# Kernel optimization log

Measured on AMD Instinct MI355X. Metric: run time of the kernel, lower is better.

Reference implementation:

```python
import jax, jax.numpy as jnp
from jax import lax
import numpy as np

NX, NQ, NU, B = 512, 512, 128, 32768
EPS = 1e-3
ALPHA = 0.0


def setup_inputs() -> dict:
    key = jax.random.key(0)
    ks = jax.random.split(key, 8)
    std = 1.0 / np.sqrt(NX)
    return {
        "t": jnp.zeros((1,), jnp.float32),
        "xi": jax.random.normal(ks[0], (B, NX), jnp.float32),
        "u": jax.random.normal(ks[1], (B, NU), jnp.float32),
        "Pstar": jax.random.normal(ks[2], (NX, NX), jnp.float32) * std,
        "Chi": jax.random.normal(ks[3], (NX, NQ), jnp.float32) * std,
        "Y1": jax.random.normal(ks[4], (NX, NX), jnp.float32) * std,
        "B2": jax.random.normal(ks[5], (NX, NU), jnp.float32) * std,
        "D12": jax.random.normal(ks[6], (NQ, NU), jnp.float32) * std,
        "X": jax.random.normal(ks[7], (NX + NQ, NX + NQ), jnp.float32) * std,
    }


def reference(t, xi, u, Pstar, Chi, Y1, B2, D12, X):
    # Parameter construction (direct parametrization of a contractive REN)
    P = 0.5 * (Pstar @ Pstar.T) + EPS * jnp.eye(NX, dtype=xi.dtype)
    H = X @ X.T + EPS * jnp.eye(NX + NQ, dtype=xi.dtype)
    H1 = H[:NX, :NX]          # [nx, nx]
    H2 = H[:NX, NX:]          # [nx, nq]
    H4 = H[NX:, NX:]          # [nq, nq]
    Y = -0.5 * (H1 + ALPHA * P + Y1 - Y1.T)
    lam = 0.5 * jnp.diagonal(H4)                 # Lambda = diag(lam)
    Pinv = jnp.linalg.inv(P)
    A = Pinv @ Y                                  # F.linear(inv(P), Y.T)
    D11 = -jnp.tril(H4, -1) / lam[:, None]        # strictly lower triangular
    C1 = Chi.T / lam[:, None]                     # [nq, nx]
    B1 = Pinv @ (-H2 - Chi)                       # [nx, nq]

    # Forward-substitution recurrence: w[:, i] = tanh(xi@C1[i] + w@D11[i] + u@D12[i])
    base = xi @ C1.T + u @ D12.T                  # [B, nq], bv = 0 (bias=False)

    def step(w, i):
        v = base[:, i] + w @ D11[i]               # [B]; D11[i, j>=i] == 0
        w = w.at[:, i].set(jnp.tanh(v))
        return w, None

    w0 = jnp.zeros((xi.shape[0], NQ), xi.dtype)
    w, _ = lax.scan(step, w0, jnp.arange(NQ))

    # xi_dot = A xi + B1 w + B2 u  (bx = 0 since bias=False)
    xi_ = xi @ A.T + w @ B1.T + u @ B2.T
    return xi_
```

## Files before the change

kernel.cpp:

```cpp
#include <hip/hip_runtime.h>
#include <hip/hip_bf16.h>
#include <cstdint>
#include <cstddef>

#define NXD 512
#define NQD 512
#define NUD 128
#define NBATCH 32768
#define EPSV 1e-3f
#define KBASE 640
#define KFIN 1152

typedef unsigned short u16;
typedef short bf16x8 __attribute__((ext_vector_type(8)));
typedef _Float16 f16x8 __attribute__((ext_vector_type(8)));
typedef float f32x4 __attribute__((ext_vector_type(4)));

__device__ __forceinline__ void gload_lds16(const u16* g, u16* l) {
  __builtin_amdgcn_global_load_lds((const __attribute__((address_space(1))) void*)g,
                                   (__attribute__((address_space(3))) void*)l, 16, 0, 0);
}

__device__ __forceinline__ float fast_tanh(float x) {
  float e = __expf(2.0f * x);
  return 1.0f - 2.0f / (e + 1.0f);
}

__device__ __forceinline__ void gbar(unsigned int* flags, unsigned int ep) {
  unsigned int* arr = flags;
  unsigned int* rel = flags + 4096;
  int tid = threadIdx.x, bid = blockIdx.x;
  __syncthreads();
  if (bid == 0) {
    if (tid == 0)
      __hip_atomic_store(&arr[0], ep, __ATOMIC_RELEASE, __HIP_MEMORY_SCOPE_AGENT);
    if (tid < 64) {
#pragma unroll
      for (int g = tid; g < 256; g += 64)
        while (__hip_atomic_load(&arr[g * 16], __ATOMIC_RELAXED, __HIP_MEMORY_SCOPE_AGENT) < ep)
          __builtin_amdgcn_s_sleep(4);
    }
    __threadfence();
    __syncthreads();
    if (tid < 64) {
#pragma unroll
      for (int g = tid; g < 256; g += 64)
        __hip_atomic_store(&rel[g * 16], ep, __ATOMIC_RELEASE, __HIP_MEMORY_SCOPE_AGENT);
    }
  } else {
    if (tid == 0) {
      __hip_atomic_store(&arr[bid * 16], ep, __ATOMIC_RELEASE, __HIP_MEMORY_SCOPE_AGENT);
      while (__hip_atomic_load(&rel[bid * 16], __ATOMIC_RELAXED, __HIP_MEMORY_SCOPE_AGENT) < ep)
        __builtin_amdgcn_s_sleep(4);
      __threadfence();
    }
    __syncthreads();
  }
}

template <int TA, int TB>
__device__ __forceinline__ void tile_mm(float acc[4][4], float* As, float* Bs,
                                        const float* A, int lda, int ai0, int ak0,
                                        const float* B, int ldb, int bj0, int bk0,
                                        int K) {
  int tid = threadIdx.x;
  int tx = tid & 15, ty = tid >> 4;
  for (int kc = 0; kc < K; kc += 16) {
    float4 av, bv;
    if (TA == 0) {
      int row = tid >> 2, q4 = (tid & 3) * 4;
      av = *(const float4*)&A[(size_t)(ai0 + row) * lda + ak0 + kc + q4];
    } else {
      int kr = tid >> 4, m4 = (tid & 15) * 4;
      av = *(const float4*)&A[(size_t)(ak0 + kc + kr) * lda + ai0 + m4];
    }
    if (TB == 0) {
      int kr = tid >> 4, j4 = (tid & 15) * 4;
      bv = *(const float4*)&B[(size_t)(bk0 + kc + kr) * ldb + bj0 + j4];
    } else {
      int row = tid >> 2, q4 = (tid & 3) * 4;
      bv = *(const float4*)&B[(size_t)(bj0 + row) * ldb + bk0 + kc + q4];
    }
    __syncthreads();
    if (TA == 0) {
      int row = tid >> 2, q4 = (tid & 3) * 4;
      As[(q4 + 0) * 68 + row] = av.x; As[(q4 + 1) * 68 + row] = av.y;
      As[(q4 + 2) * 68 + row] = av.z; As[(q4 + 3) * 68 + row] = av.w;
    } else {
      int kr = tid >> 4, m4 = (tid & 15) * 4;
      *(float4*)&As[kr * 68 + m4] = av;
    }
    if (TB == 0) {
      int kr = tid >> 4, j4 = (tid & 15) * 4;
      *(float4*)&Bs[kr * 68 + j4] = bv;
    } else {
      int row = tid >> 2, q4 = (tid & 3) * 4;
      Bs[(q4 + 0) * 68 + row] = bv.x; Bs[(q4 + 1) * 68 + row] = bv.y;
      Bs[(q4 + 2) * 68 + row] = bv.z; Bs[(q4 + 3) * 68 + row] = bv.w;
    }
    __syncthreads();
#pragma unroll
    for (int kk = 0; kk < 16; ++kk) {
      float a4[4], b4[4];
      *(float4*)a4 = *(const float4*)&As[kk * 68 + ty * 4];
      *(float4*)b4 = *(const float4*)&Bs[kk * 68 + tx * 4];
#pragma unroll
      for (int i = 0; i < 4; ++i)
#pragma unroll
        for (int j = 0; j < 4; ++j) acc[i][j] += a4[i] * b4[j];
    }
  }
}

__device__ void chol_diag64(float* Pm, int kb, float* cb2, float* Ls) {
  int tid = threadIdx.x;
  int ty = tid >> 4, tx = tid & 15;
  int base = kb * 64;
  float T[4][4];
#pragma unroll
  for (int rr = 0; rr < 4; ++rr)
#pragma unroll
    for (int cc = 0; cc < 4; ++cc)
      T[rr][cc] = Pm[(size_t)(base + ty * 4 + rr) * 512 + base + tx * 4 + cc];

  for (int c = 0; c < 64; ++c) {
    float* cb = cb2 + (c & 1) * 72;
    if (tx == (c >> 2)) {
      int cc = c & 3;
#pragma unroll
      for (int rr = 0; rr < 4; ++rr) cb[ty * 4 + rr] = T[rr][cc];
    }
    __syncthreads();
    float dcv = cb[c];
    float dc = sqrtf(dcv);
    float rdc = 1.0f / dc;
    float rdcv = 1.0f / dcv;
    if (tx == (c >> 2)) {
      int cc = c & 3;
#pragma unroll
      for (int rr = 0; rr < 4; ++rr) {
        int r = ty * 4 + rr;
        if (r == c) T[rr][cc] = dc;
        else if (r > c) T[rr][cc] *= rdc;
      }
    }
    float cr[4], cj[4];
#pragma unroll
    for (int rr = 0; rr < 4; ++rr) {
      int r = ty * 4 + rr;
      cr[rr] = (r > c) ? cb[r] * rdcv : 0.0f;
    }
#pragma unroll
    for (int cc = 0; cc < 4; ++cc) {
      int j = tx * 4 + cc;
      cj[cc] = (j > c) ? cb[j] : 0.0f;
    }
#pragma unroll
    for (int rr = 0; rr < 4; ++rr)
#pragma unroll
      for (int cc = 0; cc < 4; ++cc) T[rr][cc] -= cr[rr] * cj[cc];
  }
  __syncthreads();
#pragma unroll
  for (int rr = 0; rr < 4; ++rr)
#pragma unroll
    for (int cc = 0; cc < 4; ++cc) {
      float v = T[rr][cc];
      Pm[(size_t)(base + ty * 4 + rr) * 512 + base + tx * 4 + cc] = v;
      Ls[(ty * 4 + rr) * 64 + tx * 4 + cc] = v;
    }
  __syncthreads();
}

__device__ void diag_inv64(const float* Pm, float* Tinv, int kb, float* Ls, float* Xs) {
  int tid = threadIdx.x;
  int base = kb * 64;
  for (int idx = tid; idx < 4096; idx += 256) {
    Ls[idx] = Pm[(size_t)(base + (idx >> 6)) * 512 + base + (idx & 63)];
    Xs[idx] = 0.0f;
  }
  __syncthreads();
  if (tid < 64) {
    int j = tid;
    Xs[j * 64 + j] = 1.0f / Ls[j * 64 + j];
    for (int i = j + 1; i < 64; ++i) {
      float s = 0.0f;
      for (int k = j; k < i; ++k) s += Ls[i * 64 + k] * Xs[k * 64 + j];
      Xs[i * 64 + j] = -s / Ls[i * 64 + i];
    }
  }
  __syncthreads();
  for (int idx = tid; idx < 4096; idx += 256)
    Tinv[(size_t)(base + (idx >> 6)) * 512 + base + (idx & 63)] = Xs[idx];
  __syncthreads();
}

__global__ __launch_bounds__(256) void k_small(
    const float* __restrict__ X, const float* __restrict__ Pstar,
    const float* __restrict__ Y1, const float* __restrict__ Chi,
    const float* __restrict__ B2, const float* __restrict__ D12,
    float* __restrict__ H, float* __restrict__ Pm,
    float* __restrict__ D11, float* __restrict__ C1, float* __restrict__ Wm,
    __hip_bfloat16* __restrict__ Wbase, __hip_bfloat16* __restrict__ Wfin,
    u16* __restrict__ D11h, unsigned int* bar) {
  __shared__ float smem[8192];
  float* As = smem;
  float* Bs = smem + 1088;
  int bid = blockIdx.x;
  int tid = threadIdx.x;
  unsigned int bcnt = 0;

  float* Z1 = H;
  float* Tinv = H + 524288;
  float* Tbuf = H + 786432;

  {
    int bi = bid >> 4, bj = bid & 15;
    float acc[4][4] = {};
    tile_mm<0, 1>(acc, As, Bs, X, 1024, bi * 64, 0, X, 1024, bj * 64, 0, 1024);
    int tx = tid & 15, ty = tid >> 4;
#pragma unroll
    for (int i = 0; i < 4; ++i)
#pragma unroll
      for (int j = 0; j < 4; ++j) {
        int r = bi * 64 + ty * 4 + i, c2 = bj * 64 + tx * 4 + j;
        float v = acc[i][j];
        if (r == c2) v += EPSV;
        H[(size_t)r * 1024 + c2] = v;
      }
  }
  if (bid < 36) {
    int pi = 0, r2 = bid;
    while (r2 > pi) { r2 -= pi + 1; ++pi; }
    int pj = r2;
    float acc[4][4] = {};
    tile_mm<0, 1>(acc, As, Bs, Pstar, 512, pi * 64, 0, Pstar, 512, pj * 64, 0, 512);
    int tx = tid & 15, ty = tid >> 4;
#pragma unroll
    for (int i = 0; i < 4; ++i)
#pragma unroll
      for (int j = 0; j < 4; ++j) {
        int r = pi * 64 + ty * 4 + i, c2 = pj * 64 + tx * 4 + j;
        float v = 0.5f * acc[i][j];
        if (r == c2) v += EPSV;
        Pm[(size_t)r * 512 + c2] = v;
      }
  }
  gbar(bar, ++bcnt);

#pragma unroll
  for (int rr = 0; rr < 2; ++rr) {
    int i = bid * 2 + rr;
    float lam = 0.5f * H[(size_t)(512 + i) * 1024 + 512 + i];
    float rlam = 1.0f / lam;
    for (int j = tid; j < 512; j += 256) {
      float h4 = H[(size_t)(512 + i) * 1024 + 512 + j];
      D11[i * 512 + j] = (j < i) ? (-h4 * rlam) : 0.0f;
      C1[i * 512 + j] = Chi[(size_t)j * 512 + i] * rlam;
      float y = -0.5f * (H[(size_t)i * 1024 + j] + Y1[(size_t)i * 512 + j] - Y1[(size_t)j * 512 + i]);
      Wm[(size_t)i * 1024 + j] = y;
      Wm[(size_t)i * 1024 + 512 + j] = -H[(size_t)i * 1024 + 512 + j] - Chi[(size_t)i * 512 + j];
    }
  }
  gbar(bar, ++bcnt);

  for (int kb = 0; kb < 8; ++kb) {
    if (bid == 0) {
      chol_diag64(Pm, kb, smem + 4096, smem);
      int rem = 512 - (kb + 1) * 64;
      float* Ls = smem;
      for (int ch = 0; ch < rem; ch += 256) {
        int ir = ch + tid;
        if (ir < rem) {
          int i = (kb + 1) * 64 + ir;
          float x[64];
          float* Arow = &Pm[(size_t)i * 512 + kb * 64];
#pragma unroll
          for (int c = 0; c < 64; ++c) {
            float a0 = Arow[c], a1 = 0.f, a2 = 0.f, a3 = 0.f;
#pragma unroll
            for (int m = 0; m < c; m += 4) {
              a0 -= x[m] * Ls[c * 64 + m];
              if (m + 1 < c) a1 -= x[m + 1] * Ls[c * 64 + m + 1];
              if (m + 2 < c) a2 -= x[m + 2] * Ls[c * 64 + m + 2];
              if (m + 3 < c) a3 -= x[m + 3] * Ls[c * 64 + m + 3];
            }
            x[c] = ((a0 + a1) + (a2 + a3)) / Ls[c * 64 + c];
          }
#pragma unroll
          for (int c = 0; c < 64; ++c) Arow[c] = x[c];
        }
      }
    } else if (bid == 1 && kb > 0) {
      diag_inv64(Pm, Tinv, kb - 1, smem, smem + 4096);
    } else if (kb == 0 && bid >= 2) {
      for (int idx = (bid - 2) * 256 + tid; idx < 262144; idx += 254 * 256)
        Tinv[idx] = 0.0f;
    }
    gbar(bar, ++bcnt);

    int nr2 = 7 - kb;
    int count = nr2 * (nr2 + 1) / 2;
    if (bid < count) {
      int i = 0, r2 = bid;
      while (r2 > i) { r2 -= i + 1; ++i; }
      int j = r2;
      int p1 = (kb + 1) * 64;
      float acc[4][4] = {};
      tile_mm<0, 1>(acc, As, Bs, Pm, 512, p1 + i * 64, kb * 64,
                    Pm, 512, p1 + j * 64, kb * 64, 64);
      int tx = tid & 15, ty = tid >> 4;
#pragma unroll
      for (int ii = 0; ii < 4; ++ii)
#pragma unroll
        for (int jj = 0; jj < 4; ++jj)
          Pm[(size_t)(p1 + i * 64 + ty * 4 + ii) * 512 + p1 + j * 64 + tx * 4 + jj] -= acc[ii][jj];
    } else if (kb == 7 && bid == 0) {
      diag_inv64(Pm, Tinv, 7, smem, smem + 4096);
    }
    gbar(bar, ++bcnt);
  }

  for (int l = 0; l < 3; ++l) {
    int s = 64 << l, sd = s >> 6, tpp = sd * sd;
    int ntil = (4 >> l) * tpp;
    int p = 0, ti = 0, tj = 0;
    if (bid < ntil) {
      p = bid / tpp;
      int t = bid % tpp;
      ti = t / sd;
      tj = t % sd;
    }
    int C0 = 2 * p * s, R0 = C0 + s;
    float* Tb = Tbuf + p * s * s;
    if (bid < ntil) {
      float acc[4][4] = {};
      tile_mm<0, 0>(acc, As, Bs, Pm, 512, R0 + ti * 64, C0,
                    Tinv, 512, C0 + tj * 64, C0, s);
      int tx = tid & 15, ty = tid >> 4;
#pragma unroll
      for (int i = 0; i < 4; ++i)
#pragma unroll
        for (int j = 0; j < 4; ++j)
          Tb[(size_t)(ti * 64 + ty * 4 + i) * s + tj * 64 + tx * 4 + j] = acc[i][j];
    }
    gbar(bar, ++bcnt);
    if (bid < ntil) {
      float acc[4][4] = {};
      tile_mm<0, 0>(acc, As, Bs, Tinv, 512, R0 + ti * 64, R0,
                    Tb, s, tj * 64, 0, s);
      int tx = tid & 15, ty = tid >> 4;
#pragma unroll
      for (int i = 0; i < 4; ++i)
#pragma unroll
        for (int j = 0; j < 4; ++j)
          Tinv[(size_t)(R0 + ti * 64 + ty * 4 + i) * 512 + C0 + tj * 64 + tx * 4 + j] = -acc[i][j];
    }
    gbar(bar, ++bcnt);
  }

  {
    int ti = bid >> 4, tj = bid & 15;
    if (bid < 128) {
      float acc[4][4] = {};
      tile_mm<0, 0>(acc, As, Bs, Tinv, 512, ti * 64, 0, Wm, 1024, tj * 64, 0, 512);
      int tx = tid & 15, ty = tid >> 4;
#pragma unroll
      for (int i = 0; i < 4; ++i)
#pragma unroll
        for (int j = 0; j < 4; ++j)
          Z1[(size_t)(ti * 64 + ty * 4 + i) * 1024 + tj * 64 + tx * 4 + j] = acc[i][j];
    }
    gbar(bar, ++bcnt);
    if (bid < 128) {
      float acc[4][4] = {};
      tile_mm<1, 0>(acc, As, Bs, Tinv, 512, ti * 64, 0, Z1, 1024, tj * 64, 0, 512);
      int tx = tid & 15, ty = tid >> 4;
#pragma unroll
      for (int i = 0; i < 4; ++i)
#pragma unroll
        for (int j = 0; j < 4; ++j)
          Wm[(size_t)(ti * 64 + ty * 4 + i) * 1024 + tj * 64 + tx * 4 + j] = acc[i][j];
    }
    gbar(bar, ++bcnt);
  }

#pragma unroll
  for (int rr = 0; rr < 2; ++rr) {
    int n = bid * 2 + rr;
    for (int c = tid; c < KBASE; c += 256) {
      float v = (c < 512) ? C1[(size_t)n * 512 + c] : D12[(size_t)n * 128 + (c - 512)];
      Wbase[(size_t)n * KBASE + c] = __float2bfloat16(v);
    }
    for (int c = tid; c < KFIN; c += 256) {
      float v;
      if (c < 512) v = Wm[(size_t)n * 1024 + c];
      else if (c < 640) v = B2[(size_t)n * 128 + (c - 512)];
      else v = Wm[(size_t)n * 1024 + 512 + (c - 640)];
      Wfin[(size_t)n * KFIN + c] = __float2bfloat16(v);
    }
    for (int c = tid; c < 512; c += 256) {
      _Float16 h = (_Float16)D11[(size_t)n * 512 + c];
      D11h[(size_t)n * 512 + c] = *(u16*)&h;
    }
  }
}

__global__ __launch_bounds__(256) void k_pack_z(const float* __restrict__ xi,
                                                const float* __restrict__ u,
                                                __hip_bfloat16* __restrict__ Zb) {
  size_t b = blockIdx.x;
  for (int c = threadIdx.x; c < KBASE; c += 256) {
    float v = (c < 512) ? xi[b * 512 + c] : u[b * 128 + (c - 512)];
    Zb[b * KFIN + c] = __float2bfloat16(v);
  }
}

__global__ __launch_bounds__(256) void k_gemm_bf16(
    const u16* __restrict__ Z, int ldz,
    const u16* __restrict__ W, int ldw,
    float* __restrict__ C, int N, int K) {
  __shared__ u16 As[128 * 32];
  __shared__ u16 Bs[128 * 32];
  int tid = threadIdx.x;
  int l = tid & 63, wv = tid >> 6;
  size_t m0 = (size_t)blockIdx.x * 128;
  int n0 = blockIdx.y * 128;

  int ra = wv * 16 + (l >> 2);
  int gq = (l & 3) ^ ((l >> 2) & 3) ^ (l >> 4);
  const u16* ga0 = Z + (m0 + ra) * (size_t)ldz + gq * 8;
  const u16* ga1 = Z + (m0 + ra + 64) * (size_t)ldz + gq * 8;
  const u16* gb0 = W + (size_t)(n0 + ra) * ldw + gq * 8;
  const u16* gb1 = W + (size_t)(n0 + ra + 64) * ldw + gq * 8;
  u16* la0 = &As[wv * 512];
  u16* la1 = &As[2048 + wv * 512];
  u16* lb0 = &Bs[wv * 512];
  u16* lb1 = &Bs[2048 + wv * 512];

  int wm = (wv & 1) * 64, wn = (wv >> 1) * 64;
  int fr = l & 15;
  int fs = (l >> 4) ^ (l & 3) ^ ((l >> 2) & 3);
  int offa[4], offb[4];
#pragma unroll
  for (int t = 0; t < 4; ++t) {
    offa[t] = (wm + t * 16 + fr) * 32 + fs * 8;
    offb[t] = (wn + t * 16 + fr) * 32 + fs * 8;
  }

  f32x4 acc[4][4] = {};
  for (int k0 = 0; k0 < K; k0 += 32) {
    __syncthreads();
    gload_lds16(ga0, la0);
    gload_lds16(ga1, la1);
    gload_lds16(gb0, lb0);
    gload_lds16(gb1, lb1);
    ga0 += 32; ga1 += 32; gb0 += 32; gb1 += 32;
    __syncthreads();
    bf16x8 af[4], bfr[4];
#pragma unroll
    for (int t = 0; t < 4; ++t) {
      af[t] = *(const bf16x8*)&As[offa[t]];
      bfr[t] = *(const bf16x8*)&Bs[offb[t]];
    }
#pragma unroll
    for (int mt = 0; mt < 4; ++mt)
#pragma unroll
      for (int nt = 0; nt < 4; ++nt)
        acc[mt][nt] = __builtin_amdgcn_mfma_f32_16x16x32_bf16(af[mt], bfr[nt], acc[mt][nt], 0, 0, 0);
  }

#pragma unroll
  for (int mt = 0; mt < 4; ++mt)
#pragma unroll
    for (int nt = 0; nt < 4; ++nt) {
      int ncol = n0 + wn + nt * 16 + (l & 15);
#pragma unroll
      for (int r = 0; r < 4; ++r) {
        size_t mrow = m0 + wm + mt * 16 + (l >> 4) * 4 + r;
        C[mrow * N + ncol] = acc[mt][nt][r];
      }
    }
}

#define WSTR 520
__global__ __launch_bounds__(256) void k_scan_mfma(
    const float* __restrict__ basep,
    const float* __restrict__ D11,
    const u16* __restrict__ D11h,
    u16* __restrict__ zw) {
  __shared__ u16 wbf_s[4][16 * WSTR];
  __shared__ float ptr_s[4][16 * 16];
  __shared__ float dls_s[4][16 * 16];

  int tid = threadIdx.x;
  int wv = tid >> 6, l = tid & 63;
  int r = l & 15;
  int q = l >> 4;
  size_t gm0 = (size_t)blockIdx.x * 64 + wv * 16;

  u16* wbf = wbf_s[wv];
  float* ptr = ptr_s[wv];
  float* dls = dls_s[wv];

  float wreg[4] = {0.f, 0.f, 0.f, 0.f};

  for (int c = 0; c < 32; ++c) {
    int i0 = c * 16;
    int nk = i0 >> 5;
    int rem = c & 1;
    const u16* drow = &D11h[(size_t)(i0 + r) * 512 + q * 8];
    f16x8 bfr[16];
#pragma unroll
    for (int k = 0; k < 16; ++k)
      if (k < nk) bfr[k] = *(const f16x8*)&drow[k * 32];
    f16x8 brem = {};
    if (rem && q < 2) brem = *(const f16x8*)&drow[nk * 32];
#pragma unroll
    for (int k = 0; k < 4; ++k) {
      int ii = q + 4 * k;
      dls[ii * 16 + r] = D11[(size_t)(i0 + ii) * 512 + i0 + r];
    }
    f32x4 acc = {0.f, 0.f, 0.f, 0.f};
#pragma unroll
    for (int k = 0; k < 16; ++k)
      if (k < nk) {
        f16x8 a = *(const f16x8*)&wbf[r * WSTR + k * 32 + q * 8];
        acc = __builtin_amdgcn_mfma_f32_16x16x32_f16(a, bfr[k], acc, 0, 0, 0);
      }
    if (rem) {
      f16x8 a = {};
      if (q < 2) a = *(const f16x8*)&wbf[r * WSTR + nk * 32 + q * 8];
      acc = __builtin_amdgcn_mfma_f32_16x16x32_f16(a, brem, acc, 0, 0, 0);
    }
#pragma unroll
    for (int reg = 0; reg < 4; ++reg)
      acc[reg] += basep[(gm0 + q * 4 + reg) * 512 + i0 + r];
#pragma unroll
    for (int reg = 0; reg < 4; ++reg) {
      int m = q * 4 + reg;
      int nsw = r ^ ((m & 3) << 2);
      ptr[m * 16 + nsw] = acc[reg];
    }
    float p[16];
#pragma unroll
    for (int j = 0; j < 4; ++j) {
      float4 v4 = *(const float4*)&ptr[r * 16 + j * 4];
      int cj = (j ^ (r & 3)) * 4;
      p[cj + 0] = v4.x; p[cj + 1] = v4.y; p[cj + 2] = v4.z; p[cj + 3] = v4.w;
    }
#pragma unroll
    for (int s = 0; s < 16; ++s) {
      float prod = 0.f;
#pragma unroll
      for (int m = 0; m < 4; ++m)
        prod = fmaf(wreg[m], dls[s * 16 + q + 4 * m], prod);
      prod += __shfl_xor(prod, 16);
      prod += __shfl_xor(prod, 32);
      float w = fast_tanh(p[s] + prod);
      if ((s & 3) == q) {
        wreg[s >> 2] = w;
        *(_Float16*)&wbf[r * WSTR + i0 + s] = (_Float16)w;
      }
    }
  }
#pragma unroll
  for (int it = 0; it < 16; ++it) {
    int idx = it * 64 + l;
    int row = idx >> 6;
    int ch = idx & 63;
    f16x8 v = *(const f16x8*)&wbf[row * WSTR + ch * 8];
    u16 o[8];
#pragma unroll
    for (int e = 0; e < 8; ++e) {
      __hip_bfloat16 b = __float2bfloat16((float)v[e]);
      o[e] = *(u16*)&b;
    }
    *(uint4*)&zw[(gm0 + row) * KFIN + ch * 8] = *(const uint4*)o;
  }
}

extern "C" void kernel_launch(void* const* d_in, const int* in_sizes, int n_in,
                              void* d_out, int out_size, void* d_ws, size_t ws_size,
                              hipStream_t stream) {
  const float* xi = (const float*)d_in[1];
  const float* u = (const float*)d_in[2];
  const float* Pstar = (const float*)d_in[3];
  const float* Chi = (const float*)d_in[4];
  const float* Y1 = (const float*)d_in[5];
  const float* B2 = (const float*)d_in[6];
  const float* D12 = (const float*)d_in[7];
  const float* X = (const float*)d_in[8];
  float* out = (float*)d_out;

  char* ws = (char*)d_ws;
  __hip_bfloat16* Zb = (__hip_bfloat16*)ws;
  size_t off = (size_t)NBATCH * KFIN * sizeof(__hip_bfloat16);
  float* H = (float*)(ws + off);    off += (size_t)1024 * 1024 * 4;
  float* Pm = (float*)(ws + off);   off += (size_t)512 * 512 * 4;
  float* D11 = (float*)(ws + off);  off += (size_t)512 * 512 * 4;
  float* C1 = (float*)(ws + off);   off += (size_t)512 * 512 * 4;
  float* Wm = (float*)(ws + off);   off += (size_t)512 * 1024 * 4;
  __hip_bfloat16* Wbase = (__hip_bfloat16*)(ws + off); off += (size_t)512 * KBASE * 2;
  __hip_bfloat16* Wfin = (__hip_bfloat16*)(ws + off);  off += (size_t)512 * KFIN * 2;
  u16* D11h = (u16*)(ws + off);                        off += (size_t)512 * 512 * 2;
  unsigned int* bar = (unsigned int*)(ws + off);       off += 32768;

  (void)hipMemsetAsync(bar, 0, 32768, stream);

  k_pack_z<<<NBATCH, 256, 0, stream>>>(xi, u, Zb);

  k_small<<<256, 256, 0, stream>>>(X, Pstar, Y1, Chi, B2, D12, H, Pm,
                                   D11, C1, Wm, Wbase, Wfin, D11h, bar);

  k_gemm_bf16<<<dim3(NBATCH / 128, NQD / 128), 256, 0, stream>>>(
      (const u16*)Zb, KFIN, (const u16*)Wbase, KBASE, out, NQD, KBASE);
  k_scan_mfma<<<NBATCH / 64, 256, 0, stream>>>(out, D11, D11h, (u16*)(Zb + KBASE));
  k_gemm_bf16<<<dim3(NBATCH / 128, NXD / 128), 256, 0, stream>>>(
      (const u16*)Zb, KFIN, (const u16*)Wfin, KFIN, out, NXD, KFIN);
}
```

Before: 1.711 ms.

## Run blocked Cholesky in one block and overlap inverse with parameter prep

The blocked Cholesky and triangular-inverse phases of the parameter kernel are restructured. Block 0 now does the entire factorization and diagonal-block inversions alone with only block-local syncs, and releases per-column flags. Eight blocks then each compute one column of the inverse by blocked forward substitution, while other blocks zero the upper triangle and build D11, C1, Y and the bf16/f16 packed weights in parallel. This removes about 25 grid-wide barriers and fuses the final packing into the GEMM epilogues. In exchange the trailing update becomes serial within one block, and Wfin's memory is reused as scratch before it is written.

```diff
diff --git a/kernel.cpp b/kernel.cpp
--- a/kernel.cpp
+++ b/kernel.cpp
@@ -200,7 +200,7 @@
     const float* __restrict__ Y1, const float* __restrict__ Chi,
     const float* __restrict__ B2, const float* __restrict__ D12,
     float* __restrict__ H, float* __restrict__ Pm,
-    float* __restrict__ D11, float* __restrict__ C1, float* __restrict__ Wm,
+    float* __restrict__ D11, float* __restrict__ Tinv, float* __restrict__ Wm,
     __hip_bfloat16* __restrict__ Wbase, __hip_bfloat16* __restrict__ Wfin,
     u16* __restrict__ D11h, unsigned int* bar) {
   __shared__ float smem[8192];
@@ -208,17 +208,16 @@
   float* Bs = smem + 1088;
   int bid = blockIdx.x;
   int tid = threadIdx.x;
+  int tx = tid & 15, ty = tid >> 4;
   unsigned int bcnt = 0;
+  unsigned int* flg = bar + 8192;
 
   float* Z1 = H;
-  float* Tinv = H + 524288;
-  float* Tbuf = H + 786432;
 
   {
     int bi = bid >> 4, bj = bid & 15;
     float acc[4][4] = {};
     tile_mm<0, 1>(acc, As, Bs, X, 1024, bi * 64, 0, X, 1024, bj * 64, 0, 1024);
-    int tx = tid & 15, ty = tid >> 4;
 #pragma unroll
     for (int i = 0; i < 4; ++i)
 #pragma unroll
@@ -235,7 +234,6 @@
     int pj = r2;
     float acc[4][4] = {};
     tile_mm<0, 1>(acc, As, Bs, Pstar, 512, pi * 64, 0, Pstar, 512, pj * 64, 0, 512);
-    int tx = tid & 15, ty = tid >> 4;
 #pragma unroll
     for (int i = 0; i < 4; ++i)
 #pragma unroll
@@ -248,123 +246,122 @@
   }
   gbar(bar, ++bcnt);
 
-#pragma unroll
-  for (int rr = 0; rr < 2; ++rr) {
-    int i = bid * 2 + rr;
-    float lam = 0.5f * H[(size_t)(512 + i) * 1024 + 512 + i];
-    float rlam = 1.0f / lam;
-    for (int j = tid; j < 512; j += 256) {
-      float h4 = H[(size_t)(512 + i) * 1024 + 512 + j];
-      D11[i * 512 + j] = (j < i) ? (-h4 * rlam) : 0.0f;
-      C1[i * 512 + j] = Chi[(size_t)j * 512 + i] * rlam;
-      float y = -0.5f * (H[(size_t)i * 1024 + j] + Y1[(size_t)i * 512 + j] - Y1[(size_t)j * 512 + i]);
-      Wm[(size_t)i * 1024 + j] = y;
-      Wm[(size_t)i * 1024 + 512 + j] = -H[(size_t)i * 1024 + 512 + j] - Chi[(size_t)i * 512 + j];
-    }
-  }
-  gbar(bar, ++bcnt);
-
-  for (int kb = 0; kb < 8; ++kb) {
-    if (bid == 0) {
+  if (bid == 0) {
+    for (int kb = 0; kb < 8; ++kb) {
       chol_diag64(Pm, kb, smem + 4096, smem);
       int rem = 512 - (kb + 1) * 64;
-      float* Ls = smem;
-      for (int ch = 0; ch < rem; ch += 256) {
-        int ir = ch + tid;
-        if (ir < rem) {
-          int i = (kb + 1) * 64 + ir;
-          float x[64];
-          float* Arow = &Pm[(size_t)i * 512 + kb * 64];
-#pragma unroll
-          for (int c = 0; c < 64; ++c) {
-            float a0 = Arow[c], a1 = 0.f, a2 = 0.f, a3 = 0.f;
-#pragma unroll
-            for (int m = 0; m < c; m += 4) {
-              a0 -= x[m] * Ls[c * 64 + m];
-              if (m + 1 < c) a1 -= x[m + 1] * Ls[c * 64 + m + 1];
-              if (m + 2 < c) a2 -= x[m + 2] * Ls[c * 64 + m + 2];
-              if (m + 3 < c) a3 -= x[m + 3] * Ls[c * 64 + m + 3];
+      if (rem > 0) {
+        float* Ls = smem;
+        for (int ch = 0; ch < rem; ch += 256) {
+          int ir = ch + tid;
+          if (ir < rem) {
+            int i = (kb + 1) * 64 + ir;
+            float x[64];
+            float* Arow = &Pm[(size_t)i * 512 + kb * 64];
+#pragma unroll
+            for (int c = 0; c < 64; ++c) {
+              float a0 = Arow[c], a1 = 0.f, a2 = 0.f, a3 = 0.f;
+#pragma unroll
+              for (int m = 0; m < c; m += 4) {
+                a0 -= x[m] * Ls[c * 64 + m];
+                if (m + 1 < c) a1 -= x[m + 1] * Ls[c * 64 + m + 1];
+                if (m + 2 < c) a2 -= x[m + 2] * Ls[c * 64 + m + 2];
+                if (m + 3 < c) a3 -= x[m + 3] * Ls[c * 64 + m + 3];
+              }
+              x[c] = ((a0 + a1) + (a2 + a3)) / Ls[c * 64 + c];
             }
-            x[c] = ((a0 + a1) + (a2 + a3)) / Ls[c * 64 + c];
+#pragma unroll
+            for (int c = 0; c < 64; ++c) Arow[c] = x[c];
           }
-#pragma unroll
-          for (int c = 0; c < 64; ++c) Arow[c] = x[c];
         }
-      }
-    } else if (bid == 1 && kb > 0) {
-      diag_inv64(Pm, Tinv, kb - 1, smem, smem + 4096);
-    } else if (kb == 0 && bid >= 2) {
-      for (int idx = (bid - 2) * 256 + tid; idx < 262144; idx += 254 * 256)
-        Tinv[idx] = 0.0f;
-    }
-    gbar(bar, ++bcnt);
-
-    int nr2 = 7 - kb;
-    int count = nr2 * (nr2 + 1) / 2;
-    if (bid < count) {
-      int i = 0, r2 = bid;
-      while (r2 > i) { r2 -= i + 1; ++i; }
-      int j = r2;
+        __syncthreads();
+      }
+      diag_inv64(Pm, Tinv, kb, smem, smem + 4096);
       int p1 = (kb + 1) * 64;
+      for (int i = kb + 1; i < 8; ++i)
+        for (int j = kb + 1; j <= i; ++j) {
+          float acc[4][4] = {};
+          tile_mm<0, 1>(acc, As, Bs, Pm, 512, i * 64, kb * 64,
+                        Pm, 512, j * 64, kb * 64, 64);
+#pragma unroll
+          for (int ii = 0; ii < 4; ++ii)
+#pragma unroll
+            for (int jj = 0; jj < 4; ++jj)
+              Pm[(size_t)(i * 64 + ty * 4 + ii) * 512 + j * 64 + tx * 4 + jj] -= acc[ii][jj];
+          __syncthreads();
+        }
+      (void)p1;
+    }
+    __syncthreads();
+    if (tid == 0) {
+#pragma unroll
+      for (int r = 0; r < 8; ++r)
+        __hip_atomic_store(&flg[r * 16], 1u, __ATOMIC_RELEASE, __HIP_MEMORY_SCOPE_AGENT);
+    }
+  } else if (bid <= 8) {
+    int j = bid - 1;
+    if (tid == 0) {
+      while (__hip_atomic_load(&flg[j * 16], __ATOMIC_RELAXED, __HIP_MEMORY_SCOPE_AGENT) == 0u)
+        __builtin_amdgcn_s_sleep(8);
+      __threadfence();
+    }
+    __syncthreads();
+    float* Sb = ((float*)Wfin) + j * 4096;
+    for (int i = j + 1; i < 8; ++i) {
       float acc[4][4] = {};
-      tile_mm<0, 1>(acc, As, Bs, Pm, 512, p1 + i * 64, kb * 64,
-                    Pm, 512, p1 + j * 64, kb * 64, 64);
-      int tx = tid & 15, ty = tid >> 4;
+      tile_mm<0, 0>(acc, As, Bs, Pm, 512, i * 64, j * 64,
+                    Tinv, 512, j * 64, j * 64, (i - j) * 64);
+      __syncthreads();
 #pragma unroll
       for (int ii = 0; ii < 4; ++ii)
 #pragma unroll
         for (int jj = 0; jj < 4; ++jj)
-          Pm[(size_t)(p1 + i * 64 + ty * 4 + ii) * 512 + p1 + j * 64 + tx * 4 + jj] -= acc[ii][jj];
-    } else if (kb == 7 && bid == 0) {
-      diag_inv64(Pm, Tinv, 7, smem, smem + 4096);
-    }
-    gbar(bar, ++bcnt);
-  }
-
-  for (int l = 0; l < 3; ++l) {
-    int s = 64 << l, sd = s >> 6, tpp = sd * sd;
-    int ntil = (4 >> l) * tpp;
-    int p = 0, ti = 0, tj = 0;
-    if (bid < ntil) {
-      p = bid / tpp;
-      int t = bid % tpp;
-      ti = t / sd;
-      tj = t % sd;
-    }
-    int C0 = 2 * p * s, R0 = C0 + s;
-    float* Tb = Tbuf + p * s * s;
-    if (bid < ntil) {
-      float acc[4][4] = {};
-      tile_mm<0, 0>(acc, As, Bs, Pm, 512, R0 + ti * 64, C0,
-                    Tinv, 512, C0 + tj * 64, C0, s);
-      int tx = tid & 15, ty = tid >> 4;
-#pragma unroll
-      for (int i = 0; i < 4; ++i)
-#pragma unroll
-        for (int j = 0; j < 4; ++j)
-          Tb[(size_t)(ti * 64 + ty * 4 + i) * s + tj * 64 + tx * 4 + j] = acc[i][j];
-    }
-    gbar(bar, ++bcnt);
-    if (bid < ntil) {
-      float acc[4][4] = {};
-      tile_mm<0, 0>(acc, As, Bs, Tinv, 512, R0 + ti * 64, R0,
-                    Tb, s, tj * 64, 0, s);
-      int tx = tid & 15, ty = tid >> 4;
-#pragma unroll
-      for (int i = 0; i < 4; ++i)
-#pragma unroll
-        for (int j = 0; j < 4; ++j)
-          Tinv[(size_t)(R0 + ti * 64 + ty * 4 + i) * 512 + C0 + tj * 64 + tx * 4 + j] = -acc[i][j];
-    }
-    gbar(bar, ++bcnt);
-  }
+          Sb[(ty * 4 + ii) * 64 + tx * 4 + jj] = acc[ii][jj];
+      __syncthreads();
+      float acc2[4][4] = {};
+      tile_mm<0, 0>(acc2, As, Bs, Tinv, 512, i * 64, i * 64, Sb, 64, 0, 0, 64);
+#pragma unroll
+      for (int ii = 0; ii < 4; ++ii)
+#pragma unroll
+        for (int jj = 0; jj < 4; ++jj)
+          Tinv[(size_t)(i * 64 + ty * 4 + ii) * 512 + j * 64 + tx * 4 + jj] = -acc2[ii][jj];
+      __syncthreads();
+    }
+  } else if (bid <= 36) {
+    int t = bid - 9, i2 = 0;
+    while (t >= 7 - i2) { t -= 7 - i2; ++i2; }
+    int j2 = i2 + 1 + t;
+    for (int idx = tid; idx < 4096; idx += 256)
+      Tinv[(size_t)(i2 * 64 + (idx >> 6)) * 512 + j2 * 64 + (idx & 63)] = 0.0f;
+  } else if (bid >= 128) {
+#pragma unroll
+    for (int rr = 0; rr < 4; ++rr) {
+      int i = (bid - 128) * 4 + rr;
+      float lam = 0.5f * H[(size_t)(512 + i) * 1024 + 512 + i];
+      float rlam = 1.0f / lam;
+      for (int j = tid; j < 512; j += 256) {
+        float h4 = H[(size_t)(512 + i) * 1024 + 512 + j];
+        float d11v = (j < i) ? (-h4 * rlam) : 0.0f;
+        D11[i * 512 + j] = d11v;
+        _Float16 h = (_Float16)d11v;
+        D11h[(size_t)i * 512 + j] = *(u16*)&h;
+        float c1v = Chi[(size_t)j * 512 + i] * rlam;
+        Wbase[(size_t)i * KBASE + j] = __float2bfloat16(c1v);
+        float y = -0.5f * (H[(size_t)i * 1024 + j] + Y1[(size_t)i * 512 + j] - Y1[(size_t)j * 512 + i]);
+        Wm[(size_t)i * 1024 + j] = y;
+        Wm[(size_t)i * 1024 + 512 + j] = -H[(size_t)i * 1024 + 512 + j] - Chi[(size_t)i * 512 + j];
+      }
+      if (tid < 128)
+        Wbase[(size_t)i * KBASE + 512 + tid] = __float2bfloat16(D12[i * 128 + tid]);
+    }
+  }
+  gbar(bar, ++bcnt);
 
   {
     int ti = bid >> 4, tj = bid & 15;
     if (bid < 128) {
       float acc[4][4] = {};
       tile_mm<0, 0>(acc, As, Bs, Tinv, 512, ti * 64, 0, Wm, 1024, tj * 64, 0, 512);
-      int tx = tid & 15, ty = tid >> 4;
 #pragma unroll
       for (int i = 0; i < 4; ++i)
 #pragma unroll
@@ -375,33 +372,20 @@
     if (bid < 128) {
       float acc[4][4] = {};
       tile_mm<1, 0>(acc, As, Bs, Tinv, 512, ti * 64, 0, Z1, 1024, tj * 64, 0, 512);
-      int tx = tid & 15, ty = tid >> 4;
 #pragma unroll
       for (int i = 0; i < 4; ++i)
 #pragma unroll
-        for (int j = 0; j < 4; ++j)
-          Wm[(size_t)(ti * 64 + ty * 4 + i) * 1024 + tj * 64 + tx * 4 + j] = acc[i][j];
-    }
-    gbar(bar, ++bcnt);
-  }
-
-#pragma unroll
-  for (int rr = 0; rr < 2; ++rr) {
-    int n = bid * 2 + rr;
-    for (int c = tid; c < KBASE; c += 256) {
-      float v = (c < 512) ? C1[(size_t)n * 512 + c] : D12[(size_t)n * 128 + (c - 512)];
-      Wbase[(size_t)n * KBASE + c] = __float2bfloat16(v);
-    }
-    for (int c = tid; c < KFIN; c += 256) {
-      float v;
-      if (c < 512) v = Wm[(size_t)n * 1024 + c];
-      else if (c < 640) v = B2[(size_t)n * 128 + (c - 512)];
-      else v = Wm[(size_t)n * 1024 + 512 + (c - 640)];
-      Wfin[(size_t)n * KFIN + c] = __float2bfloat16(v);
-    }
-    for (int c = tid; c < 512; c += 256) {
-      _Float16 h = (_Float16)D11[(size_t)n * 512 + c];
-      D11h[(size_t)n * 512 + c] = *(u16*)&h;
+        for (int j = 0; j < 4; ++j) {
+          int c = tj * 64 + tx * 4 + j;
+          int wc = (c < 512) ? c : c + 128;
+          Wfin[(size_t)(ti * 64 + ty * 4 + i) * KFIN + wc] = __float2bfloat16(acc[i][j]);
+        }
+    } else if (bid < 136) {
+      int n0 = (bid - 128) * 64;
+      for (int idx = tid; idx < 64 * 128; idx += 256) {
+        int n = n0 + (idx >> 7), c = idx & 127;
+        Wfin[(size_t)n * KFIN + 512 + c] = __float2bfloat16(B2[n * 128 + c]);
+      }
     }
   }
 }
@@ -599,19 +583,19 @@
   float* H = (float*)(ws + off);    off += (size_t)1024 * 1024 * 4;
   float* Pm = (float*)(ws + off);   off += (size_t)512 * 512 * 4;
   float* D11 = (float*)(ws + off);  off += (size_t)512 * 512 * 4;
-  float* C1 = (float*)(ws + off);   off += (size_t)512 * 512 * 4;
+  float* Tinv = (float*)(ws + off); off += (size_t)512 * 512 * 4;
   float* Wm = (float*)(ws + off);   off += (size_t)512 * 1024 * 4;
   __hip_bfloat16* Wbase = (__hip_bfloat16*)(ws + off); off += (size_t)512 * KBASE * 2;
   __hip_bfloat16* Wfin = (__hip_bfloat16*)(ws + off);  off += (size_t)512 * KFIN * 2;
   u16* D11h = (u16*)(ws + off);                        off += (size_t)512 * 512 * 2;
-  unsigned int* bar = (unsigned int*)(ws + off);       off += 32768;
-
-  (void)hipMemsetAsync(bar, 0, 32768, stream);
+  unsigned int* bar = (unsigned int*)(ws + off);       off += 36864;
+
+  (void)hipMemsetAsync(bar, 0, 36864, stream);
 
   k_pack_z<<<NBATCH, 256, 0, stream>>>(xi, u, Zb);
 
   k_small<<<256, 256, 0, stream>>>(X, Pstar, Y1, Chi, B2, D12, H, Pm,
-                                   D11, C1, Wm, Wbase, Wfin, D11h, bar);
+                                   D11, Tinv, Wm, Wbase, Wfin, D11h, bar);
 
   k_gemm_bf16<<<dim3(NBATCH / 128, NQD / 128), 256, 0, stream>>>(
       (const u16*)Zb, KFIN, (const u16*)Wbase, KBASE, out, NQD, KBASE);
```

After: 2.364 ms. 38.1% more time.
